# Kernel tuning notes

Hardware: AMD Instinct MI355X
Metric: run time of the kernel (lower is better)

The kernel has to match this reference:

```python
import jax, jax.numpy as jnp
import numpy as np

H, HKV, DH = 16, 8, 128
G = H // HKV
EPS = 1e-6
ROPE_THETA = 1000000.0


def _rms_norm(x, w):
    # RMSNorm over last dim (head_dim)
    var = jnp.mean(x * x, axis=-1, keepdims=True)
    return x * jax.lax.rsqrt(var + EPS) * w


def _rotate_half(x):
    x1, x2 = jnp.split(x, 2, axis=-1)
    return jnp.concatenate([-x2, x1], axis=-1)


def setup_inputs() -> dict:
    key = jax.random.key(0)
    ks = jax.random.split(key, 5)
    B, T, D = 2, 2048, 2048
    s = 0.02
    return {
        "x": jax.random.normal(ks[0], (B, T, D), jnp.float32),
        "wq": jax.random.normal(ks[1], (H * DH, D), jnp.float32) * s,
        "wk": jax.random.normal(ks[2], (HKV * DH, D), jnp.float32) * s,
        "wv": jax.random.normal(ks[3], (HKV * DH, D), jnp.float32) * s,
        "wo": jax.random.normal(ks[4], (D, H * DH), jnp.float32) * s,
        "q_norm_w": jnp.ones((DH,), jnp.float32),
        "k_norm_w": jnp.ones((DH,), jnp.float32),
    }


def reference(x, wq, wk, wv, wo, q_norm_w, k_norm_w):
    B, T, D = x.shape
    # projections (nn.Linear: y = x @ W^T)
    q = (x @ wq.T).reshape(B, T, H, DH).transpose(0, 2, 1, 3)      # [B,H,T,Dh]
    k = (x @ wk.T).reshape(B, T, HKV, DH).transpose(0, 2, 1, 3)    # [B,Hkv,T,Dh]
    v = (x @ wv.T).reshape(B, T, HKV, DH).transpose(0, 2, 1, 3)    # [B,Hkv,T,Dh]

    # QK RMSNorm
    q = _rms_norm(q, q_norm_w)
    k = _rms_norm(k, k_norm_w)

    # RoPE (half-split style), positions 0..T-1
    inv_freq = 1.0 / (ROPE_THETA ** (jnp.arange(0, DH, 2, dtype=jnp.float32) / DH))
    freqs = jnp.arange(T, dtype=jnp.float32)[:, None] * inv_freq[None, :]   # [T,Dh/2]
    emb = jnp.concatenate([freqs, freqs], axis=-1)                           # [T,Dh]
    cos = jnp.cos(emb)[None, None, :, :]
    sin = jnp.sin(emb)[None, None, :, :]
    q = q * cos + _rotate_half(q) * sin
    k = k * cos + _rotate_half(k) * sin

    # GQA attention with fp32 scores and causal mask
    qg = q.reshape(B, HKV, G, T, DH)
    scores = jnp.einsum("bhgtd,bhkd->bhgtk", qg.astype(jnp.float32),
                        k.astype(jnp.float32)) / jnp.sqrt(jnp.float32(DH))
    causal = jnp.tril(jnp.ones((T, T), dtype=bool))[None, None, None, :, :]
    scores = jnp.where(causal, scores, jnp.finfo(jnp.float32).min)
    attn = jax.nn.softmax(scores, axis=-1).astype(x.dtype)
    ctx = jnp.einsum("bhgtk,bhkd->bhgtd", attn, v)                            # [B,Hkv,G,T,Dh]
    out = ctx.reshape(B, H, T, DH).transpose(0, 2, 1, 3).reshape(B, T, H * DH)
    return out @ wo.T
```

## Files before the change

### kernel.cpp

```cpp
#include <hip/hip_runtime.h>
#include <cstdint>

#define Hq 16
#define HKVn 8
#define DHn 128
#define Tn 2048
#define Bn 2
#define Dm 2048
#define BT (Bn*Tn)

typedef __attribute__((ext_vector_type(8))) short bfrag8;
typedef __attribute__((ext_vector_type(4))) float facc4;
typedef __attribute__((ext_vector_type(4))) _Float16 f16x4;
typedef __attribute__((ext_vector_type(8))) _Float16 f16x8;
typedef __attribute__((ext_vector_type(8))) unsigned short us8;

__device__ __forceinline__ unsigned short f2bf(float f) {
    union { float f; unsigned int u; } v; v.f = f;
    unsigned int u = v.u;
    unsigned int r = (u + 0x7FFFu + ((u >> 16) & 1u)) >> 16;
    return (unsigned short)r;
}
__device__ __forceinline__ float bf2f(unsigned short u) {
    union { unsigned int u; float f; } v; v.u = ((unsigned int)u) << 16;
    return v.f;
}

__global__ __launch_bounds__(256) void cvt_all(const float* __restrict__ x,
                                               const float* __restrict__ wq,
                                               const float* __restrict__ wk,
                                               const float* __restrict__ wv,
                                               const float* __restrict__ wo,
                                               unsigned short* __restrict__ x_bf,
                                               unsigned short* __restrict__ wqkv_bf,
                                               unsigned short* __restrict__ wo_bf,
                                               float* __restrict__ lut) {
    int i = blockIdx.x * 256 + threadIdx.x;
    if (i >= 5242880) {
        int ii = i - 5242880;
        int t = ii >> 6, d = ii & 63;
        float fr = exp2f(-(float)d * 0.3114307588956902f);
        float ang = (float)t * fr;
        float sv, cv;
        __sincosf(ang, &sv, &cv);
        lut[t * 128 + d] = cv;
        lut[t * 128 + 64 + d] = sv;
        return;
    }
    const float4* src; ushort4* dst;
    if (i < 2097152)      { src = (const float4*)x  + i;            dst = (ushort4*)x_bf + i; }
    else if (i < 3145728) { src = (const float4*)wq + (i-2097152);  dst = (ushort4*)wqkv_bf + (i-2097152); }
    else if (i < 3670016) { src = (const float4*)wk + (i-3145728);  dst = (ushort4*)wqkv_bf + 1048576 + (i-3145728); }
    else if (i < 4194304) { src = (const float4*)wv + (i-3670016);  dst = (ushort4*)wqkv_bf + 1572864 + (i-3670016); }
    else                  { src = (const float4*)wo + (i-4194304);  dst = (ushort4*)wo_bf + (i-4194304); }
    float4 v = *src;
    ushort4 y;
    y.x = f2bf(v.x); y.y = f2bf(v.y); y.z = f2bf(v.z); y.w = f2bf(v.w);
    *dst = y;
}

__device__ __forceinline__ size_t koff_tiled(int t, int d) {
    int kc = (t >> 4) & 3, l15 = t & 15;
    int f = d >> 5, qd = (d >> 3) & 3, j = d & 7;
    return (size_t)(t >> 6) * 8192 + ((((kc * 4 + f) * 64 + qd * 16 + l15) << 3) + j);
}

__global__ __launch_bounds__(256) void gemm_bt(const unsigned short* __restrict__ A,
                                               const unsigned short* __restrict__ Bm,
                                               float* __restrict__ C,
                                               int M, int N, int K) {
    __shared__ char smem[32768];
    int tid = threadIdx.x;
    int w = tid >> 6, lane = tid & 63, quad = lane >> 4, l15 = lane & 15;
    int wr = w >> 1, wc = w & 1;
    int rowBase = blockIdx.y * 128, colBase = blockIdx.x * 128;
    facc4 acc[4][4];
#pragma unroll
    for (int i = 0; i < 4; i++)
#pragma unroll
        for (int j = 0; j < 4; j++) acc[i][j] = facc4{0.f, 0.f, 0.f, 0.f};

    for (int k0 = 0; k0 < K; k0 += 64) {
        __syncthreads();
#pragma unroll
        for (int i4 = 0; i4 < 4; i4++) {
            int c = i4 * 256 + tid;
            int r = c >> 3, kkg = (c & 7) ^ (r & 7);
            const unsigned short* ga = A + (size_t)(rowBase + r) * K + k0 + kkg * 8;
            __builtin_amdgcn_global_load_lds((const __attribute__((address_space(1))) void*)ga,
                (__attribute__((address_space(3))) void*)(smem + i4 * 4096 + w * 1024), 16, 0, 0);
            const unsigned short* gb = Bm + (size_t)(colBase + r) * K + k0 + kkg * 8;
            __builtin_amdgcn_global_load_lds((const __attribute__((address_space(1))) void*)gb,
                (__attribute__((address_space(3))) void*)(smem + 16384 + i4 * 4096 + w * 1024), 16, 0, 0);
        }
        __syncthreads();
#pragma unroll
        for (int kh = 0; kh < 2; kh++) {
            bfrag8 af[4], bf[4];
#pragma unroll
            for (int i = 0; i < 4; i++) {
                int row = wr * 64 + i * 16 + l15;
                int ch = row * 8 + ((kh * 4 + quad) ^ (row & 7));
                af[i] = *(const bfrag8*)(smem + ch * 16);
            }
#pragma unroll
            for (int j = 0; j < 4; j++) {
                int row = wc * 64 + j * 16 + l15;
                int ch = row * 8 + ((kh * 4 + quad) ^ (row & 7));
                bf[j] = *(const bfrag8*)(smem + 16384 + ch * 16);
            }
#pragma unroll
            for (int i = 0; i < 4; i++)
#pragma unroll
                for (int j = 0; j < 4; j++)
                    acc[i][j] = __builtin_amdgcn_mfma_f32_16x16x32_bf16(af[i], bf[j], acc[i][j], 0, 0, 0);
        }
    }
#pragma unroll
    for (int i = 0; i < 4; i++)
#pragma unroll
        for (int j = 0; j < 4; j++)
#pragma unroll
            for (int r = 0; r < 4; r++) {
                int row = rowBase + wr * 64 + i * 16 + quad * 4 + r;
                int col = colBase + wc * 64 + j * 16 + l15;
                C[(size_t)row * N + col] = acc[i][j][r];
            }
}

__global__ __launch_bounds__(256) void gemm_qkv_fused(const unsigned short* __restrict__ A,
                                                      const unsigned short* __restrict__ Bm,
                                                      const float* __restrict__ qw,
                                                      const float* __restrict__ kw,
                                                      const float* __restrict__ lut,
                                                      unsigned short* __restrict__ q_bf,
                                                      unsigned short* __restrict__ k_bf,
                                                      _Float16* __restrict__ vT) {
    __shared__ char smem[35840];
    const int K = 2048;
    int tid = threadIdx.x;
    int w = tid >> 6, lane = tid & 63, quad = lane >> 4, l15 = lane & 15;
    int wr = w >> 1, wc = w & 1;
    int bx = blockIdx.x;
    int rowBase = blockIdx.y * 128, colBase = bx * 128;
    facc4 acc[4][4];
#pragma unroll
    for (int i = 0; i < 4; i++)
#pragma unroll
        for (int j = 0; j < 4; j++) acc[i][j] = facc4{0.f, 0.f, 0.f, 0.f};

    for (int k0 = 0; k0 < K; k0 += 64) {
        __syncthreads();
#pragma unroll
        for (int i4 = 0; i4 < 4; i4++) {
            int c = i4 * 256 + tid;
            int r = c >> 3, kkg = (c & 7) ^ (r & 7);
            const unsigned short* ga = A + (size_t)(rowBase + r) * K + k0 + kkg * 8;
            __builtin_amdgcn_global_load_lds((const __attribute__((address_space(1))) void*)ga,
                (__attribute__((address_space(3))) void*)(smem + i4 * 4096 + w * 1024), 16, 0, 0);
            const unsigned short* gb = Bm + (size_t)(colBase + r) * K + k0 + kkg * 8;
            __builtin_amdgcn_global_load_lds((const __attribute__((address_space(1))) void*)gb,
                (__attribute__((address_space(3))) void*)(smem + 16384 + i4 * 4096 + w * 1024), 16, 0, 0);
        }
        __syncthreads();
#pragma unroll
        for (int kh = 0; kh < 2; kh++) {
            bfrag8 af[4], bf[4];
#pragma unroll
            for (int i = 0; i < 4; i++) {
                int row = wr * 64 + i * 16 + l15;
                int ch = row * 8 + ((kh * 4 + quad) ^ (row & 7));
                af[i] = *(const bfrag8*)(smem + ch * 16);
            }
#pragma unroll
            for (int j = 0; j < 4; j++) {
                int row = wc * 64 + j * 16 + l15;
                int ch = row * 8 + ((kh * 4 + quad) ^ (row & 7));
                bf[j] = *(const bfrag8*)(smem + 16384 + ch * 16);
            }
#pragma unroll
            for (int i = 0; i < 4; i++)
#pragma unroll
                for (int j = 0; j < 4; j++)
                    acc[i][j] = __builtin_amdgcn_mfma_f32_16x16x32_bf16(af[i], bf[j], acc[i][j], 0, 0, 0);
        }
    }

    if (bx >= 24) {
        int hv = bx - 24;
        int gt0 = rowBase + wr * 64;
        int bb = gt0 >> 11;
        int t64 = (gt0 & 2047) >> 6;
        _Float16* base = vT + ((size_t)(bb * 8 + hv) * 32 + t64) * 8192;
#pragma unroll
        for (int i = 0; i < 4; i++) {
            int kcp = i >> 1, hh = i & 1;
#pragma unroll
            for (int j = 0; j < 4; j++) {
                int dblk = wc * 4 + j;
                f16x4 pv;
#pragma unroll
                for (int r = 0; r < 4; r++) pv[r] = (_Float16)acc[i][j][r];
                *(f16x4*)(base + (((dblk * 2 + kcp) * 64 + quad * 16 + l15) * 8) + hh * 4) = pv;
            }
        }
        return;
    }

    const float* wn = (bx < 16) ? qw : kw;
    const float osc = (bx < 16) ? (0.08838834764831845f * 1.4426950408889634f) : 1.0f;
    float* sums = (float*)(smem + 34816);
    float ssum[4][4];
#pragma unroll
    for (int i = 0; i < 4; i++)
#pragma unroll
        for (int r = 0; r < 4; r++) {
            float s = 0.f;
#pragma unroll
            for (int j = 0; j < 4; j++) s += acc[i][j][r] * acc[i][j][r];
            s += __shfl_xor(s, 1); s += __shfl_xor(s, 2);
            s += __shfl_xor(s, 4); s += __shfl_xor(s, 8);
            ssum[i][r] = s;
        }
    if (l15 == 0) {
#pragma unroll
        for (int i = 0; i < 4; i++)
#pragma unroll
            for (int r = 0; r < 4; r++)
                sums[wc * 128 + wr * 64 + i * 16 + quad * 4 + r] = ssum[i][r];
    }
    __syncthreads();
    unsigned short* tile = (unsigned short*)smem;
    float wcol[4];
#pragma unroll
    for (int j = 0; j < 4; j++) wcol[j] = wn[wc * 64 + j * 16 + l15];
#pragma unroll
    for (int i = 0; i < 4; i++)
#pragma unroll
        for (int r = 0; r < 4; r++) {
            int row = wr * 64 + i * 16 + quad * 4 + r;
            float tot = sums[row] + sums[128 + row];
            float inv = rsqrtf(tot * (1.0f / 128.0f) + 1e-6f);
#pragma unroll
            for (int j = 0; j < 4; j++)
                tile[row * 136 + wc * 64 + j * 16 + l15] = f2bf(acc[i][j][r] * inv * wcol[j]);
        }
    __syncthreads();
    {
        int row = tid >> 1, d0 = (tid & 1) * 32;
        int gt = rowBase + row;
        int t = gt & 2047, bb = gt >> 11;
        unsigned short* qrow = q_bf + ((size_t)(bb * 16 + bx) * 2048 + t) * 128;
        unsigned short* kplane = k_bf + (size_t)(bb * 8 + (bx - 16)) * 2048 * 128;
        const float* lc = lut + t * 128;
#pragma unroll
        for (int dc = 0; dc < 32; dc += 8) {
            int db = d0 + dc;
            us8 n0u = *(const us8*)(tile + row * 136 + db);
            us8 n1u = *(const us8*)(tile + row * 136 + db + 64);
            float4 cA = *(const float4*)(lc + db), cB = *(const float4*)(lc + db + 4);
            float4 sA = *(const float4*)(lc + 64 + db), sB = *(const float4*)(lc + 64 + db + 4);
            float cv[8] = {cA.x, cA.y, cA.z, cA.w, cB.x, cB.y, cB.z, cB.w};
            float sv[8] = {sA.x, sA.y, sA.z, sA.w, sB.x, sB.y, sB.z, sB.w};
            us8 p0, p1;
#pragma unroll
            for (int e = 0; e < 8; e++) {
                float a0 = bf2f(n0u[e]), a1 = bf2f(n1u[e]);
                p0[e] = f2bf((a0 * cv[e] - a1 * sv[e]) * osc);
                p1[e] = f2bf((a1 * cv[e] + a0 * sv[e]) * osc);
            }
            if (bx < 16) {
                *(us8*)(qrow + db) = p0;
                *(us8*)(qrow + db + 64) = p1;
            } else {
                *(us8*)(kplane + koff_tiled(t, db)) = p0;
                *(us8*)(kplane + koff_tiled(t, db + 64)) = p1;
            }
        }
    }
}

__global__ __launch_bounds__(256, 2) void attn_kernel(const unsigned short* __restrict__ q_bf,
                                                      const unsigned short* __restrict__ k_glob,
                                                      const _Float16* __restrict__ v_glob,
                                                      unsigned short* __restrict__ ctx) {
    __shared__ char smem[65536];
    int tid = threadIdx.x;
    int w = tid >> 6, lane = tid & 63, quad = lane >> 4, l15 = lane & 15;
    int bid = blockIdx.x;
    int u = bid & 255, halfg = bid >> 8;
    int j = u & 7, h = (u >> 3) & 15, b = (u >> 7) & 1;
    int qblk = halfg ? j : 15 - j;
    int hkv = h >> 1;
    int qb = qblk * 128;
    int qw0 = qb + w * 32;

    const unsigned short* qp = q_bf + (size_t)(b * Hq + h) * Tn * 128;
    const unsigned short* ktile = k_glob + (size_t)(b * HKVn + hkv) * 32 * 8192;
    const _Float16* vtile = v_glob + (size_t)(b * HKVn + hkv) * 32 * 8192;

    bfrag8 qf[2][4];
#pragma unroll
    for (int g = 0; g < 2; g++) {
        int row = qw0 + g * 16 + l15;
#pragma unroll
        for (int f = 0; f < 4; f++)
            qf[g][f] = *(const bfrag8*)(qp + (size_t)row * 128 + f * 32 + quad * 8);
    }

    facc4 o0[8], o1[8];
#pragma unroll
    for (int jj = 0; jj < 8; jj++) { o0[jj] = facc4{0.f,0.f,0.f,0.f}; o1[jj] = facc4{0.f,0.f,0.f,0.f}; }
    float m0 = -__builtin_inff(), m1 = -__builtin_inff(), l0 = 0.f, l1 = 0.f;

    int nkb = qb / 64 + 2;
#pragma unroll
    for (int i = 0; i < 4; i++) {
        const unsigned short* gk = ktile + (size_t)(i * 256 + tid) * 8;
        __builtin_amdgcn_global_load_lds((const __attribute__((address_space(1))) void*)gk,
            (__attribute__((address_space(3))) void*)(smem + i * 4096 + w * 1024), 16, 0, 0);
        const _Float16* gv = vtile + (size_t)(i * 256 + tid) * 8;
        __builtin_amdgcn_global_load_lds((const __attribute__((address_space(1))) void*)gv,
            (__attribute__((address_space(3))) void*)(smem + 16384 + i * 4096 + w * 1024), 16, 0, 0);
    }

    for (int ib = 0; ib < nkb; ib++) {
        int kb = ib * 64;
        __syncthreads();
        if (ib + 1 < nkb) {
            char* nb = smem + ((ib + 1) & 1) * 32768;
#pragma unroll
            for (int i = 0; i < 4; i++) {
                const unsigned short* gk = ktile + (size_t)(ib + 1) * 8192 + (i * 256 + tid) * 8;
                __builtin_amdgcn_global_load_lds((const __attribute__((address_space(1))) void*)gk,
                    (__attribute__((address_space(3))) void*)(nb + i * 4096 + w * 1024), 16, 0, 0);
                const _Float16* gv = vtile + (size_t)(ib + 1) * 8192 + (i * 256 + tid) * 8;
                __builtin_amdgcn_global_load_lds((const __attribute__((address_space(1))) void*)gv,
                    (__attribute__((address_space(3))) void*)(nb + 16384 + i * 4096 + w * 1024), 16, 0, 0);
            }
        }
        char* cb = smem + (ib & 1) * 32768;
        if (kb <= qw0 + 31) {
            facc4 s0[4], s1[4];
#pragma unroll
            for (int kc = 0; kc < 4; kc++) {
                bfrag8 kf[4];
#pragma unroll
                for (int f = 0; f < 4; f++)
                    kf[f] = *(const bfrag8*)(cb + (((kc * 4 + f) * 64 + lane) << 4));
                facc4 a = facc4{0.f,0.f,0.f,0.f}, bq = facc4{0.f,0.f,0.f,0.f};
#pragma unroll
                for (int f = 0; f < 4; f++) {
                    a  = __builtin_amdgcn_mfma_f32_16x16x32_bf16(kf[f], qf[0][f], a, 0, 0, 0);
                    bq = __builtin_amdgcn_mfma_f32_16x16x32_bf16(kf[f], qf[1][f], bq, 0, 0, 0);
                }
                s0[kc] = a; s1[kc] = bq;
            }
            if (kb + 63 > qw0) {
                int q0 = qw0 + l15, q1 = q0 + 16;
#pragma unroll
                for (int kc = 0; kc < 4; kc++)
#pragma unroll
                    for (int r = 0; r < 4; r++) {
                        int k = kb + kc * 16 + quad * 4 + r;
                        if (k > q0) s0[kc][r] = -__builtin_inff();
                        if (k > q1) s1[kc][r] = -__builtin_inff();
                    }
            }
            float mx0 = s0[0][0], mx1 = s1[0][0];
#pragma unroll
            for (int kc = 0; kc < 4; kc++)
#pragma unroll
                for (int r = 0; r < 4; r++) {
                    mx0 = fmaxf(mx0, s0[kc][r]); mx1 = fmaxf(mx1, s1[kc][r]);
                }
            mx0 = fmaxf(mx0, __shfl_xor(mx0, 16)); mx0 = fmaxf(mx0, __shfl_xor(mx0, 32));
            mx1 = fmaxf(mx1, __shfl_xor(mx1, 16)); mx1 = fmaxf(mx1, __shfl_xor(mx1, 32));
            float mn0 = fmaxf(m0, mx0), mn1 = fmaxf(m1, mx1);
            float alpha0 = exp2f(m0 - mn0), alpha1 = exp2f(m1 - mn1);
            m0 = mn0; m1 = mn1;
            float rs0 = 0.f, rs1 = 0.f;
#pragma unroll
            for (int kc = 0; kc < 4; kc++)
#pragma unroll
                for (int r = 0; r < 4; r++) {
                    s0[kc][r] = exp2f(s0[kc][r] - m0); rs0 += s0[kc][r];
                    s1[kc][r] = exp2f(s1[kc][r] - m1); rs1 += s1[kc][r];
                }
            rs0 += __shfl_xor(rs0, 16); rs0 += __shfl_xor(rs0, 32);
            rs1 += __shfl_xor(rs1, 16); rs1 += __shfl_xor(rs1, 32);
            l0 = l0 * alpha0 + rs0; l1 = l1 * alpha1 + rs1;
#pragma unroll
            for (int jj = 0; jj < 8; jj++)
#pragma unroll
                for (int r = 0; r < 4; r++) { o0[jj][r] *= alpha0; o1[jj][r] *= alpha1; }
            f16x4 pb0[4], pb1[4];
#pragma unroll
            for (int kc = 0; kc < 4; kc++) {
                pb0[kc] = f16x4{(_Float16)s0[kc][0], (_Float16)s0[kc][1],
                                (_Float16)s0[kc][2], (_Float16)s0[kc][3]};
                pb1[kc] = f16x4{(_Float16)s1[kc][0], (_Float16)s1[kc][1],
                                (_Float16)s1[kc][2], (_Float16)s1[kc][3]};
            }
#pragma unroll
            for (int kcp = 0; kcp < 2; kcp++)
#pragma unroll
                for (int dblk = 0; dblk < 8; dblk++) {
                    f16x8 vv = *(const f16x8*)(cb + 16384 + (((dblk * 2 + kcp) * 64 + lane) << 4));
                    f16x4 a0 = f16x4{vv[0], vv[1], vv[2], vv[3]};
                    f16x4 a1 = f16x4{vv[4], vv[5], vv[6], vv[7]};
                    o0[dblk] = __builtin_amdgcn_mfma_f32_16x16x16f16(a0, pb0[kcp*2],   o0[dblk], 0, 0, 0);
                    o0[dblk] = __builtin_amdgcn_mfma_f32_16x16x16f16(a1, pb0[kcp*2+1], o0[dblk], 0, 0, 0);
                    o1[dblk] = __builtin_amdgcn_mfma_f32_16x16x16f16(a0, pb1[kcp*2],   o1[dblk], 0, 0, 0);
                    o1[dblk] = __builtin_amdgcn_mfma_f32_16x16x16f16(a1, pb1[kcp*2+1], o1[dblk], 0, 0, 0);
                }
        }
    }
    float inv0 = 1.0f / l0, inv1 = 1.0f / l1;
#pragma unroll
    for (int g = 0; g < 2; g++) {
        int q = qw0 + g * 16 + l15;
        float invl = g ? inv1 : inv0;
#pragma unroll
        for (int dblk = 0; dblk < 8; dblk++) {
            facc4 ov = g ? o1[dblk] : o0[dblk];
            ushort4 st;
            st.x = f2bf(ov[0] * invl); st.y = f2bf(ov[1] * invl);
            st.z = f2bf(ov[2] * invl); st.w = f2bf(ov[3] * invl);
            *(ushort4*)(ctx + ((size_t)(b * Tn + q)) * 2048 + h * 128 + dblk * 16 + quad * 4) = st;
        }
    }
}

extern "C" void kernel_launch(void* const* d_in, const int* in_sizes, int n_in,
                              void* d_out, int out_size, void* d_ws, size_t ws_size,
                              hipStream_t stream) {
    (void)in_sizes; (void)n_in; (void)out_size; (void)ws_size;
    const float* x  = (const float*)d_in[0];
    const float* wq = (const float*)d_in[1];
    const float* wk = (const float*)d_in[2];
    const float* wv = (const float*)d_in[3];
    const float* wo = (const float*)d_in[4];
    const float* qw = (const float*)d_in[5];
    const float* kw = (const float*)d_in[6];
    float* out = (float*)d_out;
    char* ws = (char*)d_ws;

    unsigned short* x_bf    = (unsigned short*)(ws);
    unsigned short* wqkv_bf = (unsigned short*)(ws + 16777216);
    unsigned short* wo_bf   = (unsigned short*)(ws + 33554432);
    unsigned short* q_bf    = (unsigned short*)(ws + 41943040);
    unsigned short* k_bf    = (unsigned short*)(ws + 58720256);
    _Float16*       vT_f16  = (_Float16*)(ws + 67108864);
    unsigned short* ctx_bf  = (unsigned short*)(ws + 75497472);
    float*          lut     = (float*)(ws + 92274688);

    cvt_all<<<20992, 256, 0, stream>>>(x, wq, wk, wv, wo, x_bf, wqkv_bf, wo_bf, lut);
    gemm_qkv_fused<<<dim3(32, 32), 256, 0, stream>>>(x_bf, wqkv_bf, qw, kw, lut, q_bf, k_bf, vT_f16);
    attn_kernel<<<512, 256, 0, stream>>>(q_bf, k_bf, vT_f16, ctx_bf);
    gemm_bt<<<dim3(16, 32), 256, 0, stream>>>(ctx_bf, wo_bf, out, 4096, 2048, 2048);
}
```

Measured before the change: 330.2 us.

## Rewrite QKV GEMM with 256x256 tiles, double-buffered LDS and interleaved prefetch

The fused QKV projection kernel moves from 128x128 tiles with 4 waves to 256x256 tiles with 8 waves and 128KB of LDS. Each K step is split into four MFMA quadrants that overlap with async global-to-LDS loads for the next tiles, using explicit vmcnt waits, barriers, setprio and an XCD-aware block remap. The epilogue now handles two heads per block and uses a swizzled LDS tile for the norm and RoPE stage. The aim is more data reuse per block and better hiding of memory latency. The cost is heavy register and LDS pressure and tightly hand-ordered synchronisation.

```diff
diff --git a/kernel.cpp b/kernel.cpp
--- a/kernel.cpp
+++ b/kernel.cpp
@@ -128,153 +128,257 @@
             }
 }
 
-__global__ __launch_bounds__(256) void gemm_qkv_fused(const unsigned short* __restrict__ A,
-                                                      const unsigned short* __restrict__ Bm,
-                                                      const float* __restrict__ qw,
-                                                      const float* __restrict__ kw,
-                                                      const float* __restrict__ lut,
-                                                      unsigned short* __restrict__ q_bf,
-                                                      unsigned short* __restrict__ k_bf,
-                                                      _Float16* __restrict__ vT) {
-    __shared__ char smem[35840];
-    const int K = 2048;
+__device__ __forceinline__ void stage_half(const unsigned short* __restrict__ g0,
+                                           int rowBase, int k0, char* region, int h, int tid) {
+#pragma unroll
+    for (int s = 0; s < 2; s++) {
+        int c = h * 1024 + s * 512 + tid;
+        int r = c >> 3;
+        int kk = (c & 7) ^ (r & 7);
+        const unsigned short* g = g0 + (size_t)(rowBase + r) * 2048 + k0 + kk * 8;
+        __builtin_amdgcn_global_load_lds((const __attribute__((address_space(1))) void*)g,
+            (__attribute__((address_space(3))) void*)(region + c * 16), 16, 0, 0);
+    }
+}
+
+__global__ __launch_bounds__(512, 2) void gemm_qkv_fused(const unsigned short* __restrict__ A,
+                                                         const unsigned short* __restrict__ Bm,
+                                                         const float* __restrict__ qw,
+                                                         const float* __restrict__ kw,
+                                                         const float* __restrict__ lut,
+                                                         unsigned short* __restrict__ q_bf,
+                                                         unsigned short* __restrict__ k_bf,
+                                                         _Float16* __restrict__ vT) {
+    __shared__ char smem[131072];
+    const int NT = 32;
     int tid = threadIdx.x;
     int w = tid >> 6, lane = tid & 63, quad = lane >> 4, l15 = lane & 15;
-    int wr = w >> 1, wc = w & 1;
-    int bx = blockIdx.x;
-    int rowBase = blockIdx.y * 128, colBase = bx * 128;
-    facc4 acc[4][4];
-#pragma unroll
-    for (int i = 0; i < 4; i++)
-#pragma unroll
-        for (int j = 0; j < 4; j++) acc[i][j] = facc4{0.f, 0.f, 0.f, 0.f};
-
-    for (int k0 = 0; k0 < K; k0 += 64) {
-        __syncthreads();
-#pragma unroll
-        for (int i4 = 0; i4 < 4; i4++) {
-            int c = i4 * 256 + tid;
-            int r = c >> 3, kkg = (c & 7) ^ (r & 7);
-            const unsigned short* ga = A + (size_t)(rowBase + r) * K + k0 + kkg * 8;
-            __builtin_amdgcn_global_load_lds((const __attribute__((address_space(1))) void*)ga,
-                (__attribute__((address_space(3))) void*)(smem + i4 * 4096 + w * 1024), 16, 0, 0);
-            const unsigned short* gb = Bm + (size_t)(colBase + r) * K + k0 + kkg * 8;
-            __builtin_amdgcn_global_load_lds((const __attribute__((address_space(1))) void*)gb,
-                (__attribute__((address_space(3))) void*)(smem + 16384 + i4 * 4096 + w * 1024), 16, 0, 0);
-        }
-        __syncthreads();
-#pragma unroll
-        for (int kh = 0; kh < 2; kh++) {
-            bfrag8 af[4], bf[4];
-#pragma unroll
-            for (int i = 0; i < 4; i++) {
-                int row = wr * 64 + i * 16 + l15;
-                int ch = row * 8 + ((kh * 4 + quad) ^ (row & 7));
-                af[i] = *(const bfrag8*)(smem + ch * 16);
-            }
-#pragma unroll
-            for (int j = 0; j < 4; j++) {
-                int row = wc * 64 + j * 16 + l15;
-                int ch = row * 8 + ((kh * 4 + quad) ^ (row & 7));
-                bf[j] = *(const bfrag8*)(smem + 16384 + ch * 16);
-            }
-#pragma unroll
-            for (int i = 0; i < 4; i++)
-#pragma unroll
-                for (int j = 0; j < 4; j++)
-                    acc[i][j] = __builtin_amdgcn_mfma_f32_16x16x32_bf16(af[i], bf[j], acc[i][j], 0, 0, 0);
-        }
-    }
-
-    if (bx >= 24) {
-        int hv = bx - 24;
-        int gt0 = rowBase + wr * 64;
-        int bb = gt0 >> 11;
-        int t64 = (gt0 & 2047) >> 6;
-        _Float16* base = vT + ((size_t)(bb * 8 + hv) * 32 + t64) * 8192;
-#pragma unroll
-        for (int i = 0; i < 4; i++) {
-            int kcp = i >> 1, hh = i & 1;
-#pragma unroll
-            for (int j = 0; j < 4; j++) {
-                int dblk = wc * 4 + j;
-                f16x4 pv;
-#pragma unroll
-                for (int r = 0; r < 4; r++) pv[r] = (_Float16)acc[i][j][r];
-                *(f16x4*)(base + (((dblk * 2 + kcp) * 64 + quad * 16 + l15) * 8) + hh * 4) = pv;
+    int wr = w >> 2, wc = w & 3;
+    int u = ((blockIdx.x & 7) << 5) | (blockIdx.x >> 3);
+    int bx = u & 15, by = u >> 4;
+    int rowBase = by * 256, colBase = bx * 256;
+
+    facc4 acc[8][4];
+#pragma unroll
+    for (int m = 0; m < 8; m++)
+#pragma unroll
+        for (int n = 0; n < 4; n++) acc[m][n] = facc4{0.f, 0.f, 0.f, 0.f};
+
+    char* b0A = smem;           char* b0B = smem + 32768;
+    char* b1A = smem + 65536;   char* b1B = smem + 98304;
+    stage_half(A,  rowBase, 0,  b0A, 0, tid);
+    stage_half(A,  rowBase, 0,  b0A, 1, tid);
+    stage_half(Bm, colBase, 0,  b0B, 0, tid);
+    stage_half(Bm, colBase, 0,  b0B, 1, tid);
+    stage_half(A,  rowBase, 64, b1A, 0, tid);
+    stage_half(A,  rowBase, 64, b1A, 1, tid);
+    stage_half(Bm, colBase, 64, b1B, 0, tid);
+    asm volatile("s_waitcnt vmcnt(6)" ::: "memory");
+    __builtin_amdgcn_s_barrier();
+
+    for (int t = 0; t < NT; t++) {
+        __builtin_amdgcn_sched_barrier(0);
+        char* bA = smem + (t & 1) * 65536;
+        char* bB = bA + 32768;
+        char* oA = smem + ((t & 1) ^ 1) * 65536;
+        char* oB = oA + 32768;
+        int k1 = (t + 1) * 64, k2 = (t + 2) * 64;
+        bfrag8 a03[4][2], a47[4][2], b01[2][2], b23[2][2];
+
+#pragma unroll
+        for (int m = 0; m < 4; m++)
+#pragma unroll
+            for (int kh = 0; kh < 2; kh++) {
+                int row = wr * 128 + m * 16 + l15;
+                int ch = (kh * 4 + quad) ^ (row & 7);
+                a03[m][kh] = *(const bfrag8*)(bA + row * 128 + ch * 16);
+            }
+#pragma unroll
+        for (int n = 0; n < 2; n++)
+#pragma unroll
+            for (int kh = 0; kh < 2; kh++) {
+                int row = wc * 64 + n * 16 + l15;
+                int ch = (kh * 4 + quad) ^ (row & 7);
+                b01[n][kh] = *(const bfrag8*)(bB + row * 128 + ch * 16);
+            }
+        if (t + 1 < NT) stage_half(Bm, colBase, k1, oB, 1, tid);
+        __builtin_amdgcn_s_barrier();
+        asm volatile("s_waitcnt lgkmcnt(0)" ::: "memory");
+        __builtin_amdgcn_s_setprio(1);
+#pragma unroll
+        for (int m = 0; m < 4; m++)
+#pragma unroll
+            for (int n = 0; n < 2; n++)
+#pragma unroll
+                for (int kh = 0; kh < 2; kh++)
+                    acc[m][n] = __builtin_amdgcn_mfma_f32_16x16x32_bf16(a03[m][kh], b01[n][kh], acc[m][n], 0, 0, 0);
+        __builtin_amdgcn_s_setprio(0);
+        __builtin_amdgcn_s_barrier();
+
+#pragma unroll
+        for (int m = 0; m < 4; m++)
+#pragma unroll
+            for (int kh = 0; kh < 2; kh++) {
+                int row = wr * 128 + (4 + m) * 16 + l15;
+                int ch = (kh * 4 + quad) ^ (row & 7);
+                a47[m][kh] = *(const bfrag8*)(bA + row * 128 + ch * 16);
+            }
+        __builtin_amdgcn_s_barrier();
+        asm volatile("s_waitcnt lgkmcnt(0)" ::: "memory");
+        __builtin_amdgcn_s_setprio(1);
+#pragma unroll
+        for (int m = 0; m < 4; m++)
+#pragma unroll
+            for (int n = 0; n < 2; n++)
+#pragma unroll
+                for (int kh = 0; kh < 2; kh++)
+                    acc[4 + m][n] = __builtin_amdgcn_mfma_f32_16x16x32_bf16(a47[m][kh], b01[n][kh], acc[4 + m][n], 0, 0, 0);
+        __builtin_amdgcn_s_setprio(0);
+        __builtin_amdgcn_s_barrier();
+
+#pragma unroll
+        for (int n = 0; n < 2; n++)
+#pragma unroll
+            for (int kh = 0; kh < 2; kh++) {
+                int row = wc * 64 + (2 + n) * 16 + l15;
+                int ch = (kh * 4 + quad) ^ (row & 7);
+                b23[n][kh] = *(const bfrag8*)(bB + row * 128 + ch * 16);
+            }
+        if (t + 2 < NT) {
+            stage_half(A, rowBase, k2, bA, 0, tid);
+            stage_half(A, rowBase, k2, bA, 1, tid);
+        }
+        __builtin_amdgcn_s_barrier();
+        asm volatile("s_waitcnt lgkmcnt(0)" ::: "memory");
+        __builtin_amdgcn_s_setprio(1);
+#pragma unroll
+        for (int m = 0; m < 4; m++)
+#pragma unroll
+            for (int n = 0; n < 2; n++)
+#pragma unroll
+                for (int kh = 0; kh < 2; kh++)
+                    acc[4 + m][2 + n] = __builtin_amdgcn_mfma_f32_16x16x32_bf16(a47[m][kh], b23[n][kh], acc[4 + m][2 + n], 0, 0, 0);
+        __builtin_amdgcn_s_setprio(0);
+        __builtin_amdgcn_s_barrier();
+
+        if (t + 2 < NT) stage_half(Bm, colBase, k2, bB, 0, tid);
+        if (t == NT - 2)      { asm volatile("s_waitcnt vmcnt(0)" ::: "memory"); }
+        else if (t < NT - 2)  { asm volatile("s_waitcnt vmcnt(6)" ::: "memory"); }
+        __builtin_amdgcn_s_barrier();
+        __builtin_amdgcn_s_setprio(1);
+#pragma unroll
+        for (int m = 0; m < 4; m++)
+#pragma unroll
+            for (int n = 0; n < 2; n++)
+#pragma unroll
+                for (int kh = 0; kh < 2; kh++)
+                    acc[m][2 + n] = __builtin_amdgcn_mfma_f32_16x16x32_bf16(a03[m][kh], b23[n][kh], acc[m][2 + n], 0, 0, 0);
+        __builtin_amdgcn_s_setprio(0);
+        __builtin_amdgcn_s_barrier();
+    }
+
+    if (bx >= 12) {
+        int hv = (bx - 12) * 2 + (wc >> 1);
+#pragma unroll
+        for (int half = 0; half < 2; half++) {
+            int gt0 = rowBase + wr * 128 + half * 64;
+            int bb = gt0 >> 11, t64 = (gt0 & 2047) >> 6;
+            _Float16* vbase = vT + ((size_t)(bb * 8 + hv) * 32 + t64) * 8192;
+#pragma unroll
+            for (int mm = 0; mm < 4; mm++) {
+                int kcp = mm >> 1, hh = mm & 1;
+#pragma unroll
+                for (int n = 0; n < 4; n++) {
+                    int dblk = (wc & 1) * 4 + n;
+                    f16x4 pv;
+#pragma unroll
+                    for (int r = 0; r < 4; r++) pv[r] = (_Float16)acc[half * 4 + mm][n][r];
+                    *(f16x4*)(vbase + (((dblk * 2 + kcp) * 64 + quad * 16 + l15) * 8) + hh * 4) = pv;
+                }
             }
         }
         return;
     }
 
-    const float* wn = (bx < 16) ? qw : kw;
-    const float osc = (bx < 16) ? (0.08838834764831845f * 1.4426950408889634f) : 1.0f;
-    float* sums = (float*)(smem + 34816);
-    float ssum[4][4];
-#pragma unroll
-    for (int i = 0; i < 4; i++)
+    const float* wn = (bx < 8) ? qw : kw;
+    const float osc = (bx < 8) ? (0.08838834764831845f * 1.4426950408889634f) : 1.0f;
+    float* sums = (float*)smem;
+#pragma unroll
+    for (int m = 0; m < 8; m++)
 #pragma unroll
         for (int r = 0; r < 4; r++) {
             float s = 0.f;
 #pragma unroll
-            for (int j = 0; j < 4; j++) s += acc[i][j][r] * acc[i][j][r];
+            for (int n = 0; n < 4; n++) s += acc[m][n][r] * acc[m][n][r];
             s += __shfl_xor(s, 1); s += __shfl_xor(s, 2);
             s += __shfl_xor(s, 4); s += __shfl_xor(s, 8);
-            ssum[i][r] = s;
-        }
-    if (l15 == 0) {
-#pragma unroll
-        for (int i = 0; i < 4; i++)
-#pragma unroll
-            for (int r = 0; r < 4; r++)
-                sums[wc * 128 + wr * 64 + i * 16 + quad * 4 + r] = ssum[i][r];
-    }
+            if (l15 == 0) sums[wc * 256 + wr * 128 + m * 16 + quad * 4 + r] = s;
+        }
     __syncthreads();
-    unsigned short* tile = (unsigned short*)smem;
+    int hw = wc >> 1;
+    float inv[8][4];
+#pragma unroll
+    for (int m = 0; m < 8; m++)
+#pragma unroll
+        for (int r = 0; r < 4; r++) {
+            int row = wr * 128 + m * 16 + quad * 4 + r;
+            float tot = sums[(2 * hw) * 256 + row] + sums[(2 * hw + 1) * 256 + row];
+            inv[m][r] = rsqrtf(tot * (1.0f / 128.0f) + 1e-6f);
+        }
+    __syncthreads();
+    unsigned short* tileb = (unsigned short*)(smem + hw * 65536);
     float wcol[4];
 #pragma unroll
-    for (int j = 0; j < 4; j++) wcol[j] = wn[wc * 64 + j * 16 + l15];
-#pragma unroll
-    for (int i = 0; i < 4; i++)
+    for (int n = 0; n < 4; n++) wcol[n] = wn[(wc & 1) * 64 + n * 16 + l15];
+#pragma unroll
+    for (int m = 0; m < 8; m++)
 #pragma unroll
         for (int r = 0; r < 4; r++) {
-            int row = wr * 64 + i * 16 + quad * 4 + r;
-            float tot = sums[row] + sums[128 + row];
-            float inv = rsqrtf(tot * (1.0f / 128.0f) + 1e-6f);
-#pragma unroll
-            for (int j = 0; j < 4; j++)
-                tile[row * 136 + wc * 64 + j * 16 + l15] = f2bf(acc[i][j][r] * inv * wcol[j]);
+            int row = wr * 128 + m * 16 + quad * 4 + r;
+            int sw = (row & 7) << 4;
+#pragma unroll
+            for (int n = 0; n < 4; n++) {
+                int cb = ((wc & 1) * 64 + n * 16 + l15) * 2;
+                *(unsigned short*)((char*)tileb + row * 256 + (cb ^ sw)) =
+                    f2bf(acc[m][n][r] * inv[m][r] * wcol[n]);
+            }
         }
     __syncthreads();
     {
         int row = tid >> 1, d0 = (tid & 1) * 32;
         int gt = rowBase + row;
-        int t = gt & 2047, bb = gt >> 11;
-        unsigned short* qrow = q_bf + ((size_t)(bb * 16 + bx) * 2048 + t) * 128;
-        unsigned short* kplane = k_bf + (size_t)(bb * 8 + (bx - 16)) * 2048 * 128;
-        const float* lc = lut + t * 128;
-#pragma unroll
-        for (int dc = 0; dc < 32; dc += 8) {
-            int db = d0 + dc;
-            us8 n0u = *(const us8*)(tile + row * 136 + db);
-            us8 n1u = *(const us8*)(tile + row * 136 + db + 64);
-            float4 cA = *(const float4*)(lc + db), cB = *(const float4*)(lc + db + 4);
-            float4 sA = *(const float4*)(lc + 64 + db), sB = *(const float4*)(lc + 64 + db + 4);
-            float cv[8] = {cA.x, cA.y, cA.z, cA.w, cB.x, cB.y, cB.z, cB.w};
-            float sv[8] = {sA.x, sA.y, sA.z, sA.w, sB.x, sB.y, sB.z, sB.w};
-            us8 p0, p1;
-#pragma unroll
-            for (int e = 0; e < 8; e++) {
-                float a0 = bf2f(n0u[e]), a1 = bf2f(n1u[e]);
-                p0[e] = f2bf((a0 * cv[e] - a1 * sv[e]) * osc);
-                p1[e] = f2bf((a1 * cv[e] + a0 * sv[e]) * osc);
-            }
-            if (bx < 16) {
-                *(us8*)(qrow + db) = p0;
-                *(us8*)(qrow + db + 64) = p1;
-            } else {
-                *(us8*)(kplane + koff_tiled(t, db)) = p0;
-                *(us8*)(kplane + koff_tiled(t, db + 64)) = p1;
+        int tt = gt & 2047, bb = gt >> 11;
+        const float* lc = lut + tt * 128;
+        int sw = (row & 7) << 4;
+#pragma unroll
+        for (int hh2 = 0; hh2 < 2; hh2++) {
+            const char* tb = (const char*)(smem + hh2 * 65536);
+            unsigned short* qrow = 0; unsigned short* kplane = 0;
+            if (bx < 8) qrow = q_bf + ((size_t)(bb * 16 + bx * 2 + hh2) * 2048 + tt) * 128;
+            else        kplane = k_bf + (size_t)(bb * 8 + (bx - 8) * 2 + hh2) * 2048 * 128;
+#pragma unroll
+            for (int dc = 0; dc < 32; dc += 8) {
+                int db = d0 + dc;
+                us8 n0u = *(const us8*)(tb + row * 256 + ((2 * db) ^ sw));
+                us8 n1u = *(const us8*)(tb + row * 256 + ((2 * db + 128) ^ sw));
+                float4 cA = *(const float4*)(lc + db), cB = *(const float4*)(lc + db + 4);
+                float4 sA = *(const float4*)(lc + 64 + db), sB = *(const float4*)(lc + 64 + db + 4);
+                float cv[8] = {cA.x, cA.y, cA.z, cA.w, cB.x, cB.y, cB.z, cB.w};
+                float sv[8] = {sA.x, sA.y, sA.z, sA.w, sB.x, sB.y, sB.z, sB.w};
+                us8 p0, p1;
+#pragma unroll
+                for (int e = 0; e < 8; e++) {
+                    float a0 = bf2f(n0u[e]), a1 = bf2f(n1u[e]);
+                    p0[e] = f2bf((a0 * cv[e] - a1 * sv[e]) * osc);
+                    p1[e] = f2bf((a1 * cv[e] + a0 * sv[e]) * osc);
+                }
+                if (bx < 8) {
+                    *(us8*)(qrow + db) = p0;
+                    *(us8*)(qrow + db + 64) = p1;
+                } else {
+                    *(us8*)(kplane + koff_tiled(tt, db)) = p0;
+                    *(us8*)(kplane + koff_tiled(tt, db + 64)) = p1;
+                }
             }
         }
     }
@@ -456,7 +560,7 @@
     float*          lut     = (float*)(ws + 92274688);
 
     cvt_all<<<20992, 256, 0, stream>>>(x, wq, wk, wv, wo, x_bf, wqkv_bf, wo_bf, lut);
-    gemm_qkv_fused<<<dim3(32, 32), 256, 0, stream>>>(x_bf, wqkv_bf, qw, kw, lut, q_bf, k_bf, vT_f16);
+    gemm_qkv_fused<<<256, 512, 0, stream>>>(x_bf, wqkv_bf, qw, kw, lut, q_bf, k_bf, vT_f16);
     attn_kernel<<<512, 256, 0, stream>>>(q_bf, k_bf, vT_f16, ctx_bf);
     gemm_bt<<<dim3(16, 32), 256, 0, stream>>>(ctx_bf, wo_bf, out, 4096, 2048, 2048);
 }
```

Result: faster. 318.8 us (-3.5%).
